# Kernel optimization log

Measured on AMD Instinct MI355X. Metric: run time of the kernel, lower is better.

The kernel has to match this reference:

```python
import jax, jax.numpy as jnp
import numpy as np

D_MODEL = 1024
N_HEADS = 16
D_K = D_MODEL // N_HEADS


def setup_inputs() -> dict:
    key = jax.random.key(0)
    ks = jax.random.split(key, 8)
    B, S = 2, 2048
    scale = np.sqrt(2.0 / D_MODEL).astype(np.float32)
    return {
        "query": jax.random.normal(ks[0], (B, S, D_MODEL), jnp.float32),
        "key": jax.random.normal(ks[1], (B, S, D_MODEL), jnp.float32),
        "value": jax.random.normal(ks[2], (B, S, D_MODEL), jnp.float32),
        "mask": jax.random.randint(ks[3], (B, 1, S), 0, 2).astype(bool),
        "W_Q": jax.random.normal(ks[4], (D_MODEL, D_MODEL), jnp.float32) * scale,
        "W_K": jax.random.normal(ks[5], (D_MODEL, D_MODEL), jnp.float32) * scale,
        "W_V": jax.random.normal(ks[6], (D_MODEL, D_MODEL), jnp.float32) * scale,
        "W_O": jax.random.normal(ks[7], (D_MODEL, D_MODEL), jnp.float32) * scale,
    }


def reference(query, key, value, mask, W_Q, W_K, W_V, W_O):
    B, Sq, _ = query.shape
    # projections: [B, S, d_model] @ [d_model, d_model]
    def split_heads(x):  # -> [B, H, S, d_k]
        return x.reshape(B, -1, N_HEADS, D_K).transpose(0, 2, 1, 3)
    Q = split_heads(query @ W_Q)
    K = split_heads(key @ W_K)
    V = split_heads(value @ W_V)
    # scores: [B, H, Sq, Sk]
    scores = jnp.einsum("bhqd,bhkd->bhqk", Q, K) / jnp.sqrt(jnp.float32(D_K))
    m = mask[:, None, :, :]  # [B,1,1,Sk]
    scores = jnp.where(m, -jnp.inf, scores)
    attn = jax.nn.softmax(scores, axis=-1)
    out = jnp.einsum("bhqk,bhkd->bhqd", attn, V)  # [B,H,Sq,d_k]
    out = out.transpose(0, 2, 1, 3).reshape(B, Sq, D_MODEL)
    return out @ W_O
```

## Files before the change

### kernel.cpp

```cpp
#include <hip/hip_runtime.h>
#include <hip/hip_bf16.h>
#include <stdint.h>

#define DM  1024
#define SEQ 2048
#define NB  2
#define NH  16
#define DKH 64
#define SCL 0.18033688f

typedef unsigned short u16;
typedef __attribute__((ext_vector_type(8))) short short8;
typedef __attribute__((ext_vector_type(4))) float f32x4;

#define MFMA(a,b,c) __builtin_amdgcn_mfma_f32_16x16x32_bf16((a),(b),(c),0,0,0)

__device__ __forceinline__ void async_g2l16(const void* g, void* l) {
  __builtin_amdgcn_global_load_lds(
      (const __attribute__((address_space(1))) uint32_t*)g,
      (__attribute__((address_space(3))) uint32_t*)l, 16, 0, 0);
}

__device__ __forceinline__ u16 f2bf(float f) {
  uint32_t u = __builtin_bit_cast(uint32_t, f);
  u += 0x7fffu + ((u >> 16) & 1u);
  return (u16)(u >> 16);
}

__device__ __forceinline__ short8 lds_sw(const char* base, int row, int cb) {
  return *(const short8*)(base + row * 128 + (cb ^ ((row & 7) << 4)));
}

__global__ __launch_bounds__(256) void prep(
    const float* __restrict__ query, const float* __restrict__ key_,
    const float* __restrict__ value, const int* __restrict__ mask,
    const float* __restrict__ w0, const float* __restrict__ w1,
    const float* __restrict__ w2, const float* __restrict__ w3,
    u16* __restrict__ xin, u16* __restrict__ wt_qkv, u16* __restrict__ wt_o,
    int* __restrict__ idx, int* __restrict__ nkv) {
  __shared__ char shm[8320];
  const int bid = blockIdx.x;
  const int t = threadIdx.x;

  if (bid < 1024) {
    u16 (*tile)[65] = (u16(*)[65])shm;
    const int z = bid >> 8, rem = bid & 255;
    const float* W = (z == 0) ? w0 : (z == 1) ? w1 : (z == 2) ? w2 : w3;
    u16* O = (z < 3) ? (wt_qkv + (size_t)z * DM * DM) : wt_o;
    const int k0 = (rem & 15) * 64, n0 = (rem >> 4) * 64;
    const int r = t >> 2, cg = (t & 3) * 16;
    const float* src = W + (size_t)(k0 + r) * DM + n0 + cg;
#pragma unroll
    for (int j = 0; j < 4; ++j) {
      const float4 a = ((const float4*)src)[j];
      tile[r][cg + j * 4 + 0] = f2bf(a.x);
      tile[r][cg + j * 4 + 1] = f2bf(a.y);
      tile[r][cg + j * 4 + 2] = f2bf(a.z);
      tile[r][cg + j * 4 + 3] = f2bf(a.w);
    }
    __syncthreads();
    u16 u[16] __attribute__((aligned(16)));
#pragma unroll
    for (int j = 0; j < 16; ++j) u[j] = tile[cg + j][r];
    u16* dst = O + (size_t)(n0 + r) * DM + k0 + cg;
    *(uint4*)&dst[0] = *(uint4*)&u[0];
    *(uint4*)&dst[8] = *(uint4*)&u[8];
  } else if (bid < 7168) {
    const int cb = bid - 1024;
    const int z = cb >> 11;
    const float* A = (z == 0) ? query : (z == 1) ? key_ : value;
    u16* O = xin + (size_t)z * NB * SEQ * DM;
    const size_t i = (size_t)(cb & 2047) * 256 + t;
    const float4 a = ((const float4*)A)[i * 2];
    const float4 b = ((const float4*)A)[i * 2 + 1];
    u16 v[8] __attribute__((aligned(16)));
    v[0] = f2bf(a.x); v[1] = f2bf(a.y); v[2] = f2bf(a.z); v[3] = f2bf(a.w);
    v[4] = f2bf(b.x); v[5] = f2bf(b.y); v[6] = f2bf(b.z); v[7] = f2bf(b.w);
    *(uint4*)(O + i * 8) = *(uint4*)v;
  } else {
    int* cnt = (int*)shm;
    const int b = bid - 7168;
    const int* mp = mask + b * SEQ + t * 8;
    int m[8], c = 0;
#pragma unroll
    for (int j = 0; j < 8; ++j) { m[j] = mp[j]; c += (m[j] == 0); }
    cnt[t] = c;
    __syncthreads();
    for (int off = 1; off < 256; off <<= 1) {
      int v = 0;
      if (t >= off) v = cnt[t - off];
      __syncthreads();
      if (t >= off) cnt[t] += v;
      __syncthreads();
    }
    int base = cnt[t] - c;
    int* ip = idx + b * SEQ;
#pragma unroll
    for (int j = 0; j < 8; ++j)
      if (m[j] == 0) ip[base++] = t * 8 + j;
    const int total = cnt[255];
    if (t == 0) nkv[b] = total;
    for (int p = total + t; p < SEQ; p += 256) ip[p] = 0;
  }
}

__global__ __launch_bounds__(256) void kvprep(
    const u16* __restrict__ Kin, const u16* __restrict__ Vin,
    const int* __restrict__ idx, u16* __restrict__ Kc, u16* __restrict__ Vt) {
  const int bid = blockIdx.x;
  const int t = threadIdx.x;
  if (bid < 1024) {
    __shared__ u16 tile[64][65];
    const int posT = bid & 31, dmT = (bid >> 5) & 15, b = bid >> 9;
    const int r = t >> 2, cg = (t & 3) * 16;
    const int srow = idx[b * SEQ + posT * 64 + r];
    const u16* src = Vin + ((size_t)b * SEQ + srow) * DM + dmT * 64 + cg;
    u16 v[16] __attribute__((aligned(16)));
    *(uint4*)&v[0] = *(const uint4*)src;
    *(uint4*)&v[8] = *(const uint4*)(src + 8);
#pragma unroll
    for (int j = 0; j < 16; ++j) tile[r][cg + j] = v[j];
    __syncthreads();
    u16 u[16] __attribute__((aligned(16)));
#pragma unroll
    for (int j = 0; j < 16; ++j) u[j] = tile[cg + j][r];
    u16* dst = Vt + ((size_t)b * DM + dmT * 64 + r) * SEQ + posT * 64 + cg;
    *(uint4*)&dst[0] = *(uint4*)&u[0];
    *(uint4*)&dst[8] = *(uint4*)&u[8];
  } else {
    const int kb = bid - 1024;
    const int b = kb >> 6, rg = kb & 63;
    const int r = rg * 32 + (t >> 3), chunk = t & 7;
    const int srow = idx[b * SEQ + r];
    const uint4* src = (const uint4*)(Kin + ((size_t)b * SEQ + srow) * DM) + chunk;
    uint4* dst = (uint4*)(Kc + ((size_t)b * SEQ + r) * DM) + chunk;
#pragma unroll
    for (int j = 0; j < 16; ++j) dst[j * 8] = src[j * 8];
  }
}

template <int OUT_F32>
__device__ __forceinline__ void gemm128_body(
    const u16* __restrict__ A, const u16* __restrict__ Bt, void* __restrict__ Cv,
    int M, int N, int K, int bx, int by) {
  __shared__ u16 As[2][128 * 64];
  __shared__ u16 Bs[2][128 * 64];
  const int m0 = by * 128, n0 = bx * 128;
  const int t = threadIdx.x, w = t >> 6, l = t & 63;
  const int wr = w >> 1, wc = w & 1;
  const int frow = l & 15, fk8 = (l >> 4) * 8;
  f32x4 acc[4][4] = {};

  int srow[4], scb[4];
#pragma unroll
  for (int i = 0; i < 4; ++i) {
    const int T = (i * 4 + w) * 1024 + l * 16;
    srow[i] = T >> 7;
    scb[i] = (T & 127) ^ ((srow[i] & 7) << 4);
  }

#define GSTAGE(buf, k0)                                                        \
  do {                                                                         \
    _Pragma("unroll")                                                          \
    for (int i = 0; i < 4; ++i) {                                              \
      const int T = (i * 4 + w) * 1024 + l * 16;                               \
      async_g2l16((const char*)(A + (size_t)(m0 + srow[i]) * K + (k0)) + scb[i],  \
                  (char*)As[buf] + T);                                         \
      async_g2l16((const char*)(Bt + (size_t)(n0 + srow[i]) * K + (k0)) + scb[i], \
                  (char*)Bs[buf] + T);                                         \
    }                                                                          \
  } while (0)

  const int nkstep = K >> 6;
  GSTAGE(0, 0);
  __syncthreads();

  int cur = 0;
  for (int ks = 0; ks < nkstep; ++ks) {
    if (ks + 1 < nkstep) GSTAGE(cur ^ 1, (ks + 1) * 64);
    __builtin_amdgcn_s_setprio(1);
#pragma unroll
    for (int kk = 0; kk < 2; ++kk) {
      short8 af[4], bf[4];
#pragma unroll
      for (int mi = 0; mi < 4; ++mi)
        af[mi] = lds_sw((const char*)As[cur], wr * 64 + mi * 16 + frow,
                        kk * 64 + fk8 * 2);
#pragma unroll
      for (int ni = 0; ni < 4; ++ni)
        bf[ni] = lds_sw((const char*)Bs[cur], wc * 64 + ni * 16 + frow,
                        kk * 64 + fk8 * 2);
#pragma unroll
      for (int mi = 0; mi < 4; ++mi)
#pragma unroll
        for (int ni = 0; ni < 4; ++ni)
          acc[mi][ni] = MFMA(af[mi], bf[ni], acc[mi][ni]);
    }
    __builtin_amdgcn_s_setprio(0);
    __syncthreads();
    cur ^= 1;
  }
#undef GSTAGE

  const int crb = (l >> 4) * 4;
  for (int mi = 0; mi < 4; ++mi)
    for (int ni = 0; ni < 4; ++ni)
#pragma unroll
      for (int r = 0; r < 4; ++r) {
        const int row = m0 + wr * 64 + mi * 16 + crb + r;
        const int col = n0 + wc * 64 + ni * 16 + frow;
        if (OUT_F32) ((float*)Cv)[(size_t)row * N + col] = acc[mi][ni][r];
        else         ((u16*)Cv)[(size_t)row * N + col] = f2bf(acc[mi][ni][r]);
      }
}

__device__ __forceinline__ void swz256(int& bx, int& by) {
  const int lin = by * 8 + bx;
  const int s = (lin & 7) * 32 + (lin >> 3);
  bx = s & 7; by = s >> 3;
}

__global__ __launch_bounds__(256) void gemm_qkv(
    const u16* __restrict__ xin, const u16* __restrict__ wt, u16* __restrict__ out) {
  const int z = blockIdx.z;
  int bx = blockIdx.x, by = blockIdx.y;
  swz256(bx, by);
  gemm128_body<0>(xin + (size_t)z * NB * SEQ * DM, wt + (size_t)z * DM * DM,
                  out + (size_t)z * NB * SEQ * DM,
                  NB * SEQ, DM, DM, bx, by);
}

__global__ __launch_bounds__(256) void gemm_out(
    const u16* __restrict__ A, const u16* __restrict__ Bt, float* __restrict__ C) {
  int bx = blockIdx.x, by = blockIdx.y;
  swz256(bx, by);
  gemm128_body<1>(A, Bt, C, NB * SEQ, DM, DM, bx, by);
}

__global__ __launch_bounds__(512) void attn(
    const u16* __restrict__ Q, const u16* __restrict__ Kc,
    const u16* __restrict__ Vtc, const int* __restrict__ nkv,
    u16* __restrict__ O) {
  __shared__ uint4 ldsv[65536 / 16];
  char* lds = (char*)ldsv;

  const int bid = blockIdx.x;
  const int swz = (bid & 7) * 64 + (bid >> 3);
  const int qt = swz & 15, h = (swz >> 4) & 15, b = swz >> 8;
  const int t = threadIdx.x, w = t >> 6, l = t & 63;
  const int frow = l & 15, fk8 = (l >> 4) * 8, crb = (l >> 4) * 4;
  const size_t tok0 = (size_t)b * SEQ;
  const int q0 = qt * 128 + w * 16;
  const int hc = h * DKH;
  char* PW = lds + 49152 + w * 2048;

  const int nk = nkv[b];
  const int nt = (nk + 63) >> 6;

  const int T0 = w * 1024 + l * 16;
  const int r0 = T0 >> 7;
  const int c0 = (T0 & 127) ^ ((r0 & 7) << 4);
  const u16* Kg = Kc + tok0 * DM + hc;
  const u16* Vg = Vtc + ((size_t)b * DM + hc) * SEQ;

  short8 qf[2];
#pragma unroll
  for (int ks = 0; ks < 2; ++ks)
    qf[ks] = *(const short8*)(Q + (tok0 + q0 + frow) * DM + hc + ks * 32 + fk8);

  const short ONE = 0x3F80;
  const short8 ONES = {ONE, ONE, ONE, ONE, ONE, ONE, ONE, ONE};

  f32x4 o[4] = {};
  f32x4 ol = {};
  float negm[4] = {-8.f, -8.f, -8.f, -8.f};

  char* kb0 = lds;          char* kb1 = lds + 8192;   char* kb2 = lds + 16384;
  char* vb0 = lds + 24576;  char* vb1 = lds + 32768;  char* vb2 = lds + 40960;

#define STAGE(tile, kd, vd)                                                    \
  do {                                                                         \
    const int kv_ = (tile) * 64;                                               \
    async_g2l16((const char*)(Kg + (size_t)(kv_ + r0) * DM) + c0, (kd) + w * 1024); \
    async_g2l16((const char*)(Vg + (size_t)r0 * SEQ + kv_) + c0, (vd) + w * 1024);  \
  } while (0)

  if (nt > 0) STAGE(0, kb0, vb0);
  if (nt > 1) STAGE(1, kb1, vb1);

  for (int it = 0; it < nt; ++it) {
    if (it + 1 < nt) { asm volatile("s_waitcnt vmcnt(2)" ::: "memory"); }
    else             { asm volatile("s_waitcnt vmcnt(0)" ::: "memory"); }
    __builtin_amdgcn_s_barrier();
    __builtin_amdgcn_sched_barrier(0);
    if (it + 2 < nt) STAGE(it + 2, kb2, vb2);

    const int kv0 = it * 64;
    const char* Kt = kb0;
    const char* Vt = vb0;

    f32x4 s[4];
#pragma unroll
    for (int n = 0; n < 4; ++n) {
      short8 kf0 = lds_sw(Kt, n * 16 + frow, fk8 * 2);
      short8 kf1 = lds_sw(Kt, n * 16 + frow, 64 + fk8 * 2);
      f32x4 a = {};
      a = MFMA(qf[0], kf0, a);
      a = MFMA(qf[1], kf1, a);
      s[n] = a;
    }
#pragma unroll
    for (int n = 0; n < 4; ++n)
#pragma unroll
      for (int r = 0; r < 4; ++r)
        s[n][r] = __builtin_fmaf(s[n][r], SCL, negm[r]);

    if (it == nt - 1) {
#pragma unroll
      for (int n = 0; n < 4; ++n) {
        const bool valid = (kv0 + n * 16 + frow) < nk;
#pragma unroll
        for (int r = 0; r < 4; ++r)
          s[n][r] = valid ? s[n][r] : -1e30f;
      }
    }

    float lm = fmaxf(fmaxf(fmaxf(s[0][0], s[0][1]), fmaxf(s[0][2], s[0][3])),
                     fmaxf(fmaxf(s[1][0], s[1][1]), fmaxf(s[1][2], s[1][3])));
    lm = fmaxf(lm, fmaxf(fmaxf(s[2][0], s[2][1]), fmaxf(s[2][2], s[2][3])));
    lm = fmaxf(lm, fmaxf(fmaxf(s[3][0], s[3][1]), fmaxf(s[3][2], s[3][3])));
    if (__any(lm > 8.0f)) {
#pragma unroll
      for (int r = 0; r < 4; ++r) {
        float mx = fmaxf(fmaxf(s[0][r], s[1][r]), fmaxf(s[2][r], s[3][r]));
        mx = fmaxf(mx, __shfl_xor(mx, 1));
        mx = fmaxf(mx, __shfl_xor(mx, 2));
        mx = fmaxf(mx, __shfl_xor(mx, 4));
        mx = fmaxf(mx, __shfl_xor(mx, 8));
        const float d = fmaxf(mx, 0.f);
        const float al = exp2f(-d);
        negm[r] -= d;
        ol[r] *= al;
#pragma unroll
        for (int dd = 0; dd < 4; ++dd) o[dd][r] *= al;
#pragma unroll
        for (int n = 0; n < 4; ++n) s[n][r] -= d;
      }
    }

#pragma unroll
    for (int n = 0; n < 4; ++n)
#pragma unroll
      for (int r = 0; r < 4; ++r) {
        const float p = exp2f(s[n][r]);
        *(u16*)(PW + (crb + r) * 128 +
                ((n * 32 + frow * 2) ^ (((crb + r) & 7) << 4))) =
            (u16)(__builtin_bit_cast(uint32_t, p) >> 16);
      }
    asm volatile("s_waitcnt lgkmcnt(0)" ::: "memory");
    __builtin_amdgcn_sched_barrier(0);

    short8 pa0 = lds_sw(PW, frow, fk8 * 2);
    short8 pa1 = lds_sw(PW, frow, 64 + fk8 * 2);
    ol = MFMA(pa1, ONES, MFMA(pa0, ONES, ol));
#pragma unroll
    for (int d = 0; d < 4; ++d) {
      short8 vf0 = lds_sw(Vt, d * 16 + frow, fk8 * 2);
      short8 vf1 = lds_sw(Vt, d * 16 + frow, 64 + fk8 * 2);
      o[d] = MFMA(pa1, vf1, MFMA(pa0, vf0, o[d]));
    }

    char* tk = kb0; kb0 = kb1; kb1 = kb2; kb2 = tk;
    char* tv = vb0; vb0 = vb1; vb1 = vb2; vb2 = tv;
  }
#undef STAGE

#pragma unroll
  for (int r = 0; r < 4; ++r) {
    const float den = ol[r];
    const float inv = den > 0.f ? 1.f / den : 0.f;
#pragma unroll
    for (int d = 0; d < 4; ++d)
      O[(tok0 + q0 + crb + r) * DM + hc + d * 16 + frow] = f2bf(o[d][r] * inv);
  }
}

extern "C" void kernel_launch(void* const* d_in, const int* in_sizes, int n_in,
                              void* d_out, int out_size, void* d_ws, size_t ws_size,
                              hipStream_t stream) {
  const float* query = (const float*)d_in[0];
  const float* key_  = (const float*)d_in[1];
  const float* value = (const float*)d_in[2];
  const int* mask    = (const int*)d_in[3];
  const float* wq = (const float*)d_in[4];
  const float* wk = (const float*)d_in[5];
  const float* wv = (const float*)d_in[6];
  const float* wo = (const float*)d_in[7];
  float* out = (float*)d_out;
  char* ws = (char*)d_ws;

  u16* wt_qkv = (u16*)(ws);
  u16* wt_o   = (u16*)(ws + (6u << 20));
  u16* xin    = (u16*)(ws + (8u << 20));
  u16* vtc    = (u16*)(ws + (8u << 20));
  u16* attn_o = (u16*)(ws + (16u << 20));
  u16* kc     = (u16*)(ws + (24u << 20));
  u16* qkv    = (u16*)(ws + (32u << 20));
  int* idx    = (int*)(ws + (56u << 20));
  int* nkv    = (int*)(ws + (56u << 20) + 16384);

  prep<<<dim3(7170), 256, 0, stream>>>(
      query, key_, value, mask, wq, wk, wv, wo, xin, wt_qkv, wt_o, idx, nkv);

  gemm_qkv<<<dim3(DM / 128, (NB * SEQ) / 128, 3), 256, 0, stream>>>(
      xin, wt_qkv, qkv);

  kvprep<<<dim3(1152), 256, 0, stream>>>(
      qkv + (size_t)NB * SEQ * DM, qkv + (size_t)2 * NB * SEQ * DM, idx, kc, vtc);

  attn<<<dim3(NB * NH * (SEQ / 128)), 512, 0, stream>>>(
      qkv, kc, vtc, nkv, attn_o);

  gemm_out<<<dim3(DM / 128, (NB * SEQ) / 128), 256, 0, stream>>>(
      attn_o, wt_o, out);
}
```

Measured before the change: 214.5 us.

## Fuse fp32-to-bf16 input conversion into QKV GEMM A-tile loading

Removes the separate pass in prep that converted query/key/value from fp32 to bf16 into a workspace buffer. The QKV GEMM now loads fp32 A tiles into registers, converts them to bf16 and writes them into swizzled LDS after the MFMA phase, overlapping the conversion with compute. The K compaction copy in kvprep is also rearranged so each warp copies contiguous chunks of a row across more blocks. The trade is that the GEMM reads twice the A bytes through synchronous register loads instead of async global-to-LDS copies, and the rounding changes from round-to-nearest-even to round-half-up.

Result: slower. 230.2 us (+7.3%).

```diff
diff --git a/kernel.cpp b/kernel.cpp
--- a/kernel.cpp
+++ b/kernel.cpp
@@ -32,11 +32,10 @@
 }
 
 __global__ __launch_bounds__(256) void prep(
-    const float* __restrict__ query, const float* __restrict__ key_,
-    const float* __restrict__ value, const int* __restrict__ mask,
+    const int* __restrict__ mask,
     const float* __restrict__ w0, const float* __restrict__ w1,
     const float* __restrict__ w2, const float* __restrict__ w3,
-    u16* __restrict__ xin, u16* __restrict__ wt_qkv, u16* __restrict__ wt_o,
+    u16* __restrict__ wt_qkv, u16* __restrict__ wt_o,
     int* __restrict__ idx, int* __restrict__ nkv) {
   __shared__ char shm[8320];
   const int bid = blockIdx.x;
@@ -65,21 +64,9 @@
     u16* dst = O + (size_t)(n0 + r) * DM + k0 + cg;
     *(uint4*)&dst[0] = *(uint4*)&u[0];
     *(uint4*)&dst[8] = *(uint4*)&u[8];
-  } else if (bid < 7168) {
-    const int cb = bid - 1024;
-    const int z = cb >> 11;
-    const float* A = (z == 0) ? query : (z == 1) ? key_ : value;
-    u16* O = xin + (size_t)z * NB * SEQ * DM;
-    const size_t i = (size_t)(cb & 2047) * 256 + t;
-    const float4 a = ((const float4*)A)[i * 2];
-    const float4 b = ((const float4*)A)[i * 2 + 1];
-    u16 v[8] __attribute__((aligned(16)));
-    v[0] = f2bf(a.x); v[1] = f2bf(a.y); v[2] = f2bf(a.z); v[3] = f2bf(a.w);
-    v[4] = f2bf(b.x); v[5] = f2bf(b.y); v[6] = f2bf(b.z); v[7] = f2bf(b.w);
-    *(uint4*)(O + i * 8) = *(uint4*)v;
   } else {
     int* cnt = (int*)shm;
-    const int b = bid - 7168;
+    const int b = bid - 1024;
     const int* mp = mask + b * SEQ + t * 8;
     int m[8], c = 0;
 #pragma unroll
@@ -129,19 +116,20 @@
     *(uint4*)&dst[8] = *(uint4*)&u[8];
   } else {
     const int kb = bid - 1024;
-    const int b = kb >> 6, rg = kb & 63;
-    const int r = rg * 32 + (t >> 3), chunk = t & 7;
+    const int b = kb >> 8, rg = kb & 255;
+    const int r = rg * 8 + (t >> 5);
     const int srow = idx[b * SEQ + r];
-    const uint4* src = (const uint4*)(Kin + ((size_t)b * SEQ + srow) * DM) + chunk;
-    uint4* dst = (uint4*)(Kc + ((size_t)b * SEQ + r) * DM) + chunk;
-#pragma unroll
-    for (int j = 0; j < 16; ++j) dst[j * 8] = src[j * 8];
-  }
-}
-
-template <int OUT_F32>
+    const int co = (t & 31) * 4;
+    const uint4* src = (const uint4*)(Kin + ((size_t)b * SEQ + srow) * DM);
+    uint4* dst = (uint4*)(Kc + ((size_t)b * SEQ + r) * DM);
+#pragma unroll
+    for (int j = 0; j < 4; ++j) dst[co + j] = src[co + j];
+  }
+}
+
+template <int A_F32, int OUT_F32>
 __device__ __forceinline__ void gemm128_body(
-    const u16* __restrict__ A, const u16* __restrict__ Bt, void* __restrict__ Cv,
+    const void* __restrict__ Av, const u16* __restrict__ Bt, void* __restrict__ Cv,
     int M, int N, int K, int bx, int by) {
   __shared__ u16 As[2][128 * 64];
   __shared__ u16 Bs[2][128 * 64];
@@ -149,6 +137,8 @@
   const int t = threadIdx.x, w = t >> 6, l = t & 63;
   const int wr = w >> 1, wc = w & 1;
   const int frow = l & 15, fk8 = (l >> 4) * 8;
+  const u16* Ab = (const u16*)Av;
+  const float* Af = (const float*)Av;
   f32x4 acc[4][4] = {};
 
   int srow[4], scb[4];
@@ -159,25 +149,64 @@
     scb[i] = (T & 127) ^ ((srow[i] & 7) << 4);
   }
 
-#define GSTAGE(buf, k0)                                                        \
+  float4 av[8];
+
+#define ISSUE_B(buf, k0)                                                       \
   do {                                                                         \
     _Pragma("unroll")                                                          \
-    for (int i = 0; i < 4; ++i) {                                              \
-      const int T = (i * 4 + w) * 1024 + l * 16;                               \
-      async_g2l16((const char*)(A + (size_t)(m0 + srow[i]) * K + (k0)) + scb[i],  \
-                  (char*)As[buf] + T);                                         \
+    for (int i = 0; i < 4; ++i)                                                \
       async_g2l16((const char*)(Bt + (size_t)(n0 + srow[i]) * K + (k0)) + scb[i], \
-                  (char*)Bs[buf] + T);                                         \
+                  (char*)Bs[buf] + (i * 4 + w) * 1024);                        \
+  } while (0)
+
+#define ISSUE_A16(buf, k0)                                                     \
+  do {                                                                         \
+    _Pragma("unroll")                                                          \
+    for (int i = 0; i < 4; ++i)                                                \
+      async_g2l16((const char*)(Ab + (size_t)(m0 + srow[i]) * K + (k0)) + scb[i], \
+                  (char*)As[buf] + (i * 4 + w) * 1024);                        \
+  } while (0)
+
+#define ISSUE_A32(k0)                                                          \
+  do {                                                                         \
+    _Pragma("unroll")                                                          \
+    for (int c = 0; c < 8; ++c) {                                              \
+      const int idx_ = c * 256 + t;                                            \
+      av[c] = *(const float4*)(Af + (size_t)(m0 + (idx_ >> 4)) * K + (k0) +    \
+                               (idx_ & 15) * 4);                               \
     }                                                                          \
   } while (0)
 
-  const int nkstep = K >> 6;
-  GSTAGE(0, 0);
+#define WRITE_A32(buf)                                                         \
+  do {                                                                         \
+    _Pragma("unroll")                                                          \
+    for (int c = 0; c < 8; ++c) {                                              \
+      const int idx_ = c * 256 + t;                                            \
+      const int row_ = idx_ >> 4, c4_ = idx_ & 15;                             \
+      uint32_t u0 = __builtin_bit_cast(uint32_t, av[c].x) + 0x8000u;           \
+      uint32_t u1 = __builtin_bit_cast(uint32_t, av[c].y) + 0x8000u;           \
+      uint32_t u2 = __builtin_bit_cast(uint32_t, av[c].z) + 0x8000u;           \
+      uint32_t u3 = __builtin_bit_cast(uint32_t, av[c].w) + 0x8000u;           \
+      uint2 pk;                                                                \
+      pk.x = (u1 & 0xFFFF0000u) | (u0 >> 16);                                  \
+      pk.y = (u3 & 0xFFFF0000u) | (u2 >> 16);                                  \
+      *(uint2*)((char*)As[buf] + row_ * 128 + ((c4_ * 8) ^ ((row_ & 7) << 4))) = pk; \
+    }                                                                          \
+  } while (0)
+
+  const int nks = K >> 6;
+  if (A_F32) { ISSUE_A32(0); } else { ISSUE_A16(0, 0); }
+  ISSUE_B(0, 0);
+  if (A_F32) WRITE_A32(0);
   __syncthreads();
 
   int cur = 0;
-  for (int ks = 0; ks < nkstep; ++ks) {
-    if (ks + 1 < nkstep) GSTAGE(cur ^ 1, (ks + 1) * 64);
+  for (int ks = 0; ks < nks; ++ks) {
+    const bool more = (ks + 1 < nks);
+    if (more) {
+      if (A_F32) { ISSUE_A32((ks + 1) * 64); } else { ISSUE_A16(cur ^ 1, (ks + 1) * 64); }
+      ISSUE_B(cur ^ 1, (ks + 1) * 64);
+    }
     __builtin_amdgcn_s_setprio(1);
 #pragma unroll
     for (int kk = 0; kk < 2; ++kk) {
@@ -197,10 +226,14 @@
           acc[mi][ni] = MFMA(af[mi], bf[ni], acc[mi][ni]);
     }
     __builtin_amdgcn_s_setprio(0);
+    if (more && A_F32) WRITE_A32(cur ^ 1);
     __syncthreads();
     cur ^= 1;
   }
-#undef GSTAGE
+#undef ISSUE_B
+#undef ISSUE_A16
+#undef ISSUE_A32
+#undef WRITE_A32
 
   const int crb = (l >> 4) * 4;
   for (int mi = 0; mi < 4; ++mi)
@@ -221,20 +254,23 @@
 }
 
 __global__ __launch_bounds__(256) void gemm_qkv(
-    const u16* __restrict__ xin, const u16* __restrict__ wt, u16* __restrict__ out) {
+    const float* __restrict__ query, const float* __restrict__ key_,
+    const float* __restrict__ value, const u16* __restrict__ wt,
+    u16* __restrict__ out) {
   const int z = blockIdx.z;
+  const float* A = (z == 0) ? query : (z == 1) ? key_ : value;
   int bx = blockIdx.x, by = blockIdx.y;
   swz256(bx, by);
-  gemm128_body<0>(xin + (size_t)z * NB * SEQ * DM, wt + (size_t)z * DM * DM,
-                  out + (size_t)z * NB * SEQ * DM,
-                  NB * SEQ, DM, DM, bx, by);
+  gemm128_body<1, 0>(A, wt + (size_t)z * DM * DM,
+                     out + (size_t)z * NB * SEQ * DM,
+                     NB * SEQ, DM, DM, bx, by);
 }
 
 __global__ __launch_bounds__(256) void gemm_out(
     const u16* __restrict__ A, const u16* __restrict__ Bt, float* __restrict__ C) {
   int bx = blockIdx.x, by = blockIdx.y;
   swz256(bx, by);
-  gemm128_body<1>(A, Bt, C, NB * SEQ, DM, DM, bx, by);
+  gemm128_body<0, 1>(A, Bt, C, NB * SEQ, DM, DM, bx, by);
 }
 
 __global__ __launch_bounds__(512) void attn(
@@ -401,7 +437,6 @@
 
   u16* wt_qkv = (u16*)(ws);
   u16* wt_o   = (u16*)(ws + (6u << 20));
-  u16* xin    = (u16*)(ws + (8u << 20));
   u16* vtc    = (u16*)(ws + (8u << 20));
   u16* attn_o = (u16*)(ws + (16u << 20));
   u16* kc     = (u16*)(ws + (24u << 20));
@@ -409,13 +444,13 @@
   int* idx    = (int*)(ws + (56u << 20));
   int* nkv    = (int*)(ws + (56u << 20) + 16384);
 
-  prep<<<dim3(7170), 256, 0, stream>>>(
-      query, key_, value, mask, wq, wk, wv, wo, xin, wt_qkv, wt_o, idx, nkv);
+  prep<<<dim3(1026), 256, 0, stream>>>(
+      mask, wq, wk, wv, wo, wt_qkv, wt_o, idx, nkv);
 
   gemm_qkv<<<dim3(DM / 128, (NB * SEQ) / 128, 3), 256, 0, stream>>>(
-      xin, wt_qkv, qkv);
-
-  kvprep<<<dim3(1152), 256, 0, stream>>>(
+      query, key_, value, wt_qkv, qkv);
+
+  kvprep<<<dim3(1536), 256, 0, stream>>>(
       qkv + (size_t)NB * SEQ * DM, qkv + (size_t)2 * NB * SEQ * DM, idx, kc, vtc);
 
   attn<<<dim3(NB * NH * (SEQ / 128)), 512, 0, stream>>>(
```
